# Kernel optimization log

Measured on AMD Instinct MI355X. Metric: run time of the kernel, lower is better.

The kernel has to match this reference:

```python
import jax, jax.numpy as jnp
import numpy as np

NUM_HEADS = 4


def setup_inputs() -> dict:
    key = jax.random.key(0)
    ks = jax.random.split(key, 14)
    B, T, N, Fin, Fout, E = 4, 16, 1000, 64, 128, 12000
    s_in = 1.0 / np.sqrt(Fin)
    s_out = 1.0 / np.sqrt(Fout)
    return {
        "x": jax.random.normal(ks[0], (B, T, N, Fin), jnp.float32),
        "edge_index": jax.random.randint(ks[1], (2, E), 0, N, dtype=jnp.int64),
        # per-gate ChebConv weights (gate order: z, r, h); W0 = self term, W1 = neighbor term
        "wx0": jax.random.normal(ks[2], (3, Fin, Fout), jnp.float32) * s_in,
        "wx1": jax.random.normal(ks[3], (3, Fin, Fout), jnp.float32) * s_in,
        "bx": jax.random.normal(ks[4], (3, Fout), jnp.float32) * 0.01,
        "wh0": jax.random.normal(ks[5], (3, Fout, Fout), jnp.float32) * s_out,
        "wh1": jax.random.normal(ks[6], (3, Fout, Fout), jnp.float32) * s_out,
        "bh": jax.random.normal(ks[7], (3, Fout), jnp.float32) * 0.01,
        # torch nn.MultiheadAttention params
        "w_in": jax.random.normal(ks[8], (3 * Fout, Fout), jnp.float32) * s_out,
        "b_in": jax.random.normal(ks[9], (3 * Fout,), jnp.float32) * 0.01,
        "w_out": jax.random.normal(ks[10], (Fout, Fout), jnp.float32) * s_out,
        "b_out": jax.random.normal(ks[11], (Fout,), jnp.float32) * 0.01,
    }


def reference(x, edge_index, wx0, wx1, bx, wh0, wh1, bh, w_in, b_in, w_out, b_out):
    B, T, N, Fin = x.shape
    Fout = wx0.shape[-1]
    H = NUM_HEADS
    Dh = Fout // H
    L = B * T
    row, col = edge_index[0], edge_index[1]

    # symmetric normalization  D^{-1/2} A D^{-1/2}
    deg = jax.ops.segment_sum(jnp.ones(row.shape, x.dtype), row, num_segments=N)
    dinv = jnp.where(deg > 0, 1.0 / jnp.sqrt(jnp.maximum(deg, 1.0)), 0.0)
    normw = dinv[row] * dinv[col]  # [E]

    # [B,T,N,F] -> [N, T*B, F]  (time-major merge, matching x.view in torch)
    xg = x.transpose(2, 1, 0, 3).reshape(N, T * B, Fin)

    def conv(z, W0, W1, b):
        # ChebConv-style: self transform + sym-normalized 1-hop aggregation
        agg = jax.ops.segment_sum(normw[:, None, None] * z[col], row, num_segments=N)
        return z @ W0 + agg @ W1 + b

    # single GConvGRU step with H0 = 0
    h0 = jnp.zeros((N, T * B, Fout), x.dtype)
    Z = jax.nn.sigmoid(conv(xg, wx0[0], wx1[0], bx[0]) + conv(h0, wh0[0], wh1[0], bh[0]))
    R = jax.nn.sigmoid(conv(xg, wx0[1], wx1[1], bx[1]) + conv(h0, wh0[1], wh1[1], bh[1]))
    Ht = jnp.tanh(conv(xg, wx0[2], wx1[2], bx[2]) + conv(h0 * R, wh0[2], wh1[2], bh[2]))
    Hn = Z * h0 + (1.0 - Z) * Ht  # [N, T*B, Fout]

    # [N,T*B,F] -> [B*T, N, F]  (torch MHA layout: L=B*T, batch=N)
    a = Hn.reshape(N, T, B, Fout).transpose(2, 1, 0, 3).reshape(L, N, Fout)
    qkv = a @ w_in.T + b_in
    q, k, v = jnp.split(qkv, 3, axis=-1)

    def heads(t):
        return t.reshape(L, N, H, Dh).transpose(1, 2, 0, 3)  # [N,H,L,Dh]

    q, k, v = heads(q), heads(k), heads(v)
    att = jax.nn.softmax(jnp.einsum('nhld,nhmd->nhlm', q, k) / np.sqrt(Dh).astype(x.dtype), axis=-1)
    ctx = jnp.einsum('nhlm,nhmd->nhld', att, v).transpose(2, 0, 1, 3).reshape(L, N, Fout)
    out = ctx @ w_out.T + b_out
    return out.reshape(B, T, N, Fout)
```

## Files before the change

### kernel.cpp

```cpp
#include <hip/hip_runtime.h>
#include <math.h>

#define Nn 1000

#define OFF_ROWPTR 0
#define OFF_CSCOL  2048
#define OFF_CSW    18432
#define OFF_WCAT   34816
#define OFF_BC     67584
#define OFF_WTIN   67840
#define OFF_WTOUT  116992
#define OFF_XGAT   133376
#define OFF_Q      8325376
#define OFF_KV     16517376
#define OFF_END    32901376

__global__ __launch_bounds__(1024)
void k_csr(const void* edge, int E, int* rowptr_g, int* cs_col, float* cs_w) {
  __shared__ int deg[1000];
  __shared__ int rp[1001];
  __shared__ int fill[1000];
  __shared__ float dinv[1000];
  __shared__ int sflag;
  __shared__ int sc[1024];
  const int tid = threadIdx.x;
  if (tid == 0) {
    const long long* p = (const long long*)edge;
    int ok = 1;
    for (int i = 0; i < 16; ++i) { long long v = p[i]; if (v < 0 || v >= Nn) ok = 0; }
    sflag = ok;
  }
  for (int i = tid; i < 1000; i += 1024) { deg[i] = 0; fill[i] = 0; }
  __syncthreads();
  const int fl = sflag;
  for (int e = tid; e < E; e += 1024) {
    int r = fl ? (int)((const long long*)edge)[e] : ((const int*)edge)[e];
    atomicAdd(&deg[r], 1);
  }
  __syncthreads();
  sc[tid] = (tid < 1000) ? deg[tid] : 0;
  __syncthreads();
  for (int off = 1; off < 1024; off <<= 1) {
    int t = (tid >= off) ? sc[tid - off] : 0;
    __syncthreads();
    sc[tid] += t;
    __syncthreads();
  }
  if (tid == 0) { rp[0] = 0; rowptr_g[0] = 0; }
  if (tid < 1000) {
    rp[tid + 1] = sc[tid];
    rowptr_g[tid + 1] = sc[tid];
    float d = (float)deg[tid];
    dinv[tid] = (d > 0.f) ? (1.0f / sqrtf(d)) : 0.f;
  }
  __syncthreads();
  for (int e = tid; e < E; e += 1024) {
    int r = fl ? (int)((const long long*)edge)[e] : ((const int*)edge)[e];
    int c = fl ? (int)((const long long*)edge)[E + e] : ((const int*)edge)[E + e];
    int pos = rp[r] + atomicAdd(&fill[r], 1);
    cs_col[pos] = c;
    cs_w[pos] = dinv[r] * dinv[c];
  }
}

__global__ __launch_bounds__(256)
void k_prep(const float* __restrict__ x,
            const float* __restrict__ wx0, const float* __restrict__ wx1,
            const float* __restrict__ bx, const float* __restrict__ bh,
            const float* __restrict__ w_in, const float* __restrict__ w_out,
            float* __restrict__ ws) {
  const int bid = blockIdx.x;
  const int tid = threadIdx.x;
  if (bid < 1000) {
    __shared__ float tile[64][65];
    const int n = bid;
    const int f = tid & 63;
    #pragma unroll
    for (int i = 0; i < 16; ++i) {
      const int bt = (tid >> 6) + i * 4;
      const int l = (bt & 15) * 4 + (bt >> 4);
      tile[f][l] = x[(bt * 1000 + n) * 64 + f];
    }
    __syncthreads();
    const int l = tid & 63;
    #pragma unroll
    for (int i = 0; i < 16; ++i) {
      const int fo = (tid >> 6) + i * 4;
      ws[OFF_XGAT + n * 4096 + fo * 64 + l] = tile[fo][l];
    }
    return;
  }
  int idx = (bid - 1000) * 256 + tid;
  if (idx < 32768) {
    int f = idx >> 8, j = idx & 255;
    int g = (j < 128) ? 0 : 2, jj = j & 127;
    float v = (f < 64) ? wx0[(g * 64 + f) * 128 + jj]
                       : wx1[(g * 64 + (f - 64)) * 128 + jj];
    ws[OFF_WCAT + idx] = v;
    return;
  }
  idx -= 32768;
  if (idx < 256) {
    int g = (idx < 128) ? 0 : 2, jj = idx & 127;
    ws[OFF_BC + idx] = bx[g * 128 + jj] + bh[g * 128 + jj];
    return;
  }
  idx -= 256;
  if (idx < 49152) {
    int f = idx / 384, j = idx % 384;
    ws[OFF_WTIN + idx] = w_in[j * 128 + f];
    return;
  }
  idx -= 49152;
  if (idx < 16384) {
    int f = idx >> 7, j = idx & 127;
    ws[OFF_WTOUT + idx] = w_out[j * 128 + f];
  }
}

__global__ __launch_bounds__(256, 4)
void k_fused2(const float* __restrict__ ws, const int* __restrict__ wsi,
              float* __restrict__ out,
              const float* __restrict__ b_in, const float* __restrict__ b_out,
              float* __restrict__ qs_base, float* __restrict__ kv_base) {
  __shared__ float lds[8192];
  const int n = blockIdx.x;
  const int tid = threadIdx.x;
  float* __restrict__ qs = qs_base + (size_t)n * 8192;
  float* __restrict__ kv = kv_base + (size_t)n * 16384;

  {
    const float4* xsrc = reinterpret_cast<const float4*>(ws + OFF_XGAT + n * 4096);
    #pragma unroll
    for (int i = 0; i < 4; ++i)
      *reinterpret_cast<float4*>(lds + 4096 + i * 1024 + tid * 4) = xsrc[i * 256 + tid];
    float4 acc[4];
    #pragma unroll
    for (int i = 0; i < 4; ++i) { acc[i].x = 0.f; acc[i].y = 0.f; acc[i].z = 0.f; acc[i].w = 0.f; }
    const int kb = wsi[OFF_ROWPTR + n], ke = wsi[OFF_ROWPTR + n + 1];
    for (int k = kb; k < ke; ++k) {
      const int c = wsi[OFF_CSCOL + k];
      const float wgt = ws[OFF_CSW + k];
      const float4* src = reinterpret_cast<const float4*>(ws + OFF_XGAT + c * 4096);
      #pragma unroll
      for (int i = 0; i < 4; ++i) {
        const float4 v = src[i * 256 + tid];
        acc[i].x = fmaf(wgt, v.x, acc[i].x);
        acc[i].y = fmaf(wgt, v.y, acc[i].y);
        acc[i].z = fmaf(wgt, v.z, acc[i].z);
        acc[i].w = fmaf(wgt, v.w, acc[i].w);
      }
    }
    #pragma unroll
    for (int i = 0; i < 4; ++i)
      *reinterpret_cast<float4*>(lds + i * 1024 + tid * 4) = acc[i];
  }
  __syncthreads();

  const int ry = tid >> 5, tx = tid & 31;
  const int r0 = ry * 8, j0 = tx * 4;

  {
    float accz[8][4], acch[8][4];
    #pragma unroll
    for (int c = 0; c < 4; ++c) {
      const float bz = ws[OFF_BC + j0 + c];
      const float bhv = ws[OFF_BC + 128 + j0 + c];
      #pragma unroll
      for (int r = 0; r < 8; ++r) { accz[r][c] = bz; acch[r][c] = bhv; }
    }
    const float* Wc = ws + OFF_WCAT;
    #pragma unroll 2
    for (int f = 0; f < 128; ++f) {
      const int base = (f < 64) ? (4096 + f * 64) : ((f - 64) * 64);
      const float4 a0 = *reinterpret_cast<const float4*>(lds + base + r0);
      const float4 a1 = *reinterpret_cast<const float4*>(lds + base + r0 + 4);
      const float4 wz = *reinterpret_cast<const float4*>(Wc + f * 256 + j0);
      const float4 wh = *reinterpret_cast<const float4*>(Wc + f * 256 + 128 + j0);
      const float av[8] = {a0.x, a0.y, a0.z, a0.w, a1.x, a1.y, a1.z, a1.w};
      const float wzv[4] = {wz.x, wz.y, wz.z, wz.w};
      const float whv[4] = {wh.x, wh.y, wh.z, wh.w};
      #pragma unroll
      for (int r = 0; r < 8; ++r)
        #pragma unroll
        for (int c = 0; c < 4; ++c) {
          accz[r][c] = fmaf(av[r], wzv[c], accz[r][c]);
          acch[r][c] = fmaf(av[r], whv[c], acch[r][c]);
        }
    }
    __syncthreads();
    #pragma unroll
    for (int r = 0; r < 8; ++r) {
      const int l = r0 + r;
      const int lp = (l & 3) * 16 + (l >> 2);
      float4 v;
      const float z0 = 1.0f / (1.0f + __expf(-accz[r][0]));
      const float z1 = 1.0f / (1.0f + __expf(-accz[r][1]));
      const float z2 = 1.0f / (1.0f + __expf(-accz[r][2]));
      const float z3 = 1.0f / (1.0f + __expf(-accz[r][3]));
      v.x = (1.0f - z0) * tanhf(acch[r][0]);
      v.y = (1.0f - z1) * tanhf(acch[r][1]);
      v.z = (1.0f - z2) * tanhf(acch[r][2]);
      v.w = (1.0f - z3) * tanhf(acch[r][3]);
      *reinterpret_cast<float4*>(lds + lp * 128 + j0) = v;
    }
  }
  __syncthreads();

  {
    const float* Wt = ws + OFF_WTIN;
    #pragma unroll
    for (int g = 0; g < 3; ++g) {
      float acc[8][4];
      #pragma unroll
      for (int c = 0; c < 4; ++c) {
        const float b = b_in[g * 128 + j0 + c];
        #pragma unroll
        for (int r = 0; r < 8; ++r) acc[r][c] = b;
      }
      #pragma unroll 1
      for (int fc = 0; fc < 32; ++fc) {
        float av[8][4];
        #pragma unroll
        for (int r = 0; r < 8; ++r)
          *reinterpret_cast<float4*>(av[r]) =
              *reinterpret_cast<const float4*>(lds + (r0 + r) * 128 + fc * 4);
        #pragma unroll
        for (int i = 0; i < 4; ++i) {
          const float4 w4 = *reinterpret_cast<const float4*>(Wt + (fc * 4 + i) * 384 + g * 128 + j0);
          const float wv[4] = {w4.x, w4.y, w4.z, w4.w};
          #pragma unroll
          for (int r = 0; r < 8; ++r)
            #pragma unroll
            for (int c = 0; c < 4; ++c)
              acc[r][c] = fmaf(av[r][i], wv[c], acc[r][c]);
        }
      }
      if (g == 0) {
        #pragma unroll
        for (int r = 0; r < 8; ++r)
          #pragma unroll
          for (int c = 0; c < 4; ++c)
            qs[(j0 + c) * 64 + (r0 + r)] = acc[r][c];
      } else {
        float* dst = kv + (g - 1) * 8192;
        #pragma unroll
        for (int r = 0; r < 8; ++r) {
          float4 v;
          v.x = acc[r][0]; v.y = acc[r][1]; v.z = acc[r][2]; v.w = acc[r][3];
          *reinterpret_cast<float4*>(dst + (r0 + r) * 128 + j0) = v;
        }
      }
    }
  }
  __syncthreads();

  {
    const int h = tid >> 6, l = tid & 63;
    float q[32];
    #pragma unroll
    for (int d = 0; d < 32; ++d)
      q[d] = qs[(h * 32 + d) * 64 + l] * 0.17677669529663687f;
    float den = 0.f;
    float cx[32];
    #pragma unroll
    for (int d = 0; d < 32; ++d) cx[d] = 0.f;
    #pragma unroll 2
    for (int m = 0; m < 64; ++m) {
      const float* kr = kv + m * 128 + h * 32;
      float s0 = 0.f, s1 = 0.f, s2 = 0.f, s3 = 0.f;
      #pragma unroll
      for (int i = 0; i < 8; ++i) {
        const float4 kvv = *reinterpret_cast<const float4*>(kr + i * 4);
        s0 = fmaf(q[i * 4 + 0], kvv.x, s0);
        s1 = fmaf(q[i * 4 + 1], kvv.y, s1);
        s2 = fmaf(q[i * 4 + 2], kvv.z, s2);
        s3 = fmaf(q[i * 4 + 3], kvv.w, s3);
      }
      const float p = __expf((s0 + s1) + (s2 + s3));
      den += p;
      const float* vr = kv + 8192 + m * 128 + h * 32;
      #pragma unroll
      for (int i = 0; i < 8; ++i) {
        const float4 vv = *reinterpret_cast<const float4*>(vr + i * 4);
        cx[i * 4 + 0] = fmaf(p, vv.x, cx[i * 4 + 0]);
        cx[i * 4 + 1] = fmaf(p, vv.y, cx[i * 4 + 1]);
        cx[i * 4 + 2] = fmaf(p, vv.z, cx[i * 4 + 2]);
        cx[i * 4 + 3] = fmaf(p, vv.w, cx[i * 4 + 3]);
      }
    }
    const float inv = 1.0f / den;
    const int ms = (l & 7) << 2;
    #pragma unroll
    for (int i = 0; i < 8; ++i) {
      float4 v;
      v.x = cx[i * 4 + 0] * inv; v.y = cx[i * 4 + 1] * inv;
      v.z = cx[i * 4 + 2] * inv; v.w = cx[i * 4 + 3] * inv;
      *reinterpret_cast<float4*>(lds + l * 128 + ((h * 32 + i * 4) ^ ms)) = v;
    }
  }
  __syncthreads();

  {
    float acc[8][4];
    #pragma unroll
    for (int c = 0; c < 4; ++c) {
      const float b = b_out[j0 + c];
      #pragma unroll
      for (int r = 0; r < 8; ++r) acc[r][c] = b;
    }
    const float* Wt = ws + OFF_WTOUT;
    #pragma unroll 1
    for (int fc = 0; fc < 32; ++fc) {
      float av[8][4];
      #pragma unroll
      for (int r = 0; r < 8; ++r) {
        const int row = r0 + r;
        const int ms = (row & 7) << 2;
        *reinterpret_cast<float4*>(av[r]) =
            *reinterpret_cast<const float4*>(lds + row * 128 + ((fc * 4) ^ ms));
      }
      #pragma unroll
      for (int i = 0; i < 4; ++i) {
        const float4 w4 = *reinterpret_cast<const float4*>(Wt + (fc * 4 + i) * 128 + j0);
        const float wv[4] = {w4.x, w4.y, w4.z, w4.w};
        #pragma unroll
        for (int r = 0; r < 8; ++r)
          #pragma unroll
          for (int c = 0; c < 4; ++c)
            acc[r][c] = fmaf(av[r][i], wv[c], acc[r][c]);
      }
    }
    #pragma unroll
    for (int r = 0; r < 8; ++r) {
      float4 v;
      v.x = acc[r][0]; v.y = acc[r][1]; v.z = acc[r][2]; v.w = acc[r][3];
      *reinterpret_cast<float4*>(out + ((size_t)((r0 + r) * 1000 + n)) * 128 + j0) = v;
    }
  }
}

__global__ __launch_bounds__(1024, 1)
void k_fused(const float* __restrict__ ws, const int* __restrict__ wsi,
             float* __restrict__ out,
             const float* __restrict__ b_in, const float* __restrict__ b_out) {
  extern __shared__ float lds[];
  float* R_X = lds;
  float* R_A = lds + 8192;
  float* R_K = lds + 16384;
  float* R_V = lds + 24576;
  float* WL  = lds + 16384;
  const int n = blockIdx.x;
  const int tid = threadIdx.x;
  const int lane = tid & 63;
  const int w = tid >> 6;

  {
    const int f = tid >> 4, l4 = tid & 15;
    const float4 xv = *reinterpret_cast<const float4*>(ws + OFF_XGAT + n * 4096 + f * 64 + l4 * 4);
    *reinterpret_cast<float4*>(R_X + f * 64 + l4 * 4) = xv;
    const int kb = wsi[OFF_ROWPTR + n], ke = wsi[OFF_ROWPTR + n + 1];
    float4 acc = {0.f, 0.f, 0.f, 0.f};
    for (int k = kb; k < ke; ++k) {
      const int c = wsi[OFF_CSCOL + k];
      const float wgt = ws[OFF_CSW + k];
      const float4 v = *reinterpret_cast<const float4*>(ws + OFF_XGAT + c * 4096 + f * 64 + l4 * 4);
      acc.x = fmaf(wgt, v.x, acc.x);
      acc.y = fmaf(wgt, v.y, acc.y);
      acc.z = fmaf(wgt, v.z, acc.z);
      acc.w = fmaf(wgt, v.w, acc.w);
    }
    *reinterpret_cast<float4*>(R_X + (64 + f) * 64 + l4 * 4) = acc;
  }
  __syncthreads();

  {
    float accz[8], acch[8];
    #pragma unroll
    for (int c = 0; c < 8; ++c) {
      accz[c] = ws[OFF_BC + w * 8 + c];
      acch[c] = ws[OFF_BC + 128 + w * 8 + c];
    }
    for (int ch = 0; ch < 2; ++ch) {
      const float4* src = reinterpret_cast<const float4*>(ws + OFF_WCAT + ch * 16384);
      float4* dst = reinterpret_cast<float4*>(WL);
      #pragma unroll
      for (int i = 0; i < 4; ++i) dst[tid + i * 1024] = src[tid + i * 1024];
      __syncthreads();
      #pragma unroll 4
      for (int f0 = 0; f0 < 64; ++f0) {
        const float av = R_X[(ch * 64 + f0) * 64 + lane];
        const float4 wz0 = *reinterpret_cast<const float4*>(WL + f0 * 256 + w * 8);
        const float4 wz1 = *reinterpret_cast<const float4*>(WL + f0 * 256 + w * 8 + 4);
        const float4 wh0 = *reinterpret_cast<const float4*>(WL + f0 * 256 + 128 + w * 8);
        const float4 wh1 = *reinterpret_cast<const float4*>(WL + f0 * 256 + 128 + w * 8 + 4);
        accz[0] = fmaf(av, wz0.x, accz[0]); accz[1] = fmaf(av, wz0.y, accz[1]);
        accz[2] = fmaf(av, wz0.z, accz[2]); accz[3] = fmaf(av, wz0.w, accz[3]);
        accz[4] = fmaf(av, wz1.x, accz[4]); accz[5] = fmaf(av, wz1.y, accz[5]);
        accz[6] = fmaf(av, wz1.z, accz[6]); accz[7] = fmaf(av, wz1.w, accz[7]);
        acch[0] = fmaf(av, wh0.x, acch[0]); acch[1] = fmaf(av, wh0.y, acch[1]);
        acch[2] = fmaf(av, wh0.z, acch[2]); acch[3] = fmaf(av, wh0.w, acch[3]);
        acch[4] = fmaf(av, wh1.x, acch[4]); acch[5] = fmaf(av, wh1.y, acch[5]);
        acch[6] = fmaf(av, wh1.z, acch[6]); acch[7] = fmaf(av, wh1.w, acch[7]);
      }
      __syncthreads();
    }
    #pragma unroll
    for (int c = 0; c < 8; ++c) {
      const float z = 1.0f / (1.0f + __expf(-accz[c]));
      const float hn = (1.0f - z) * tanhf(acch[c]);
      R_A[(w * 8 + c) * 64 + lane] = hn;
    }
  }
  __syncthreads();

  {
    float acc[24];
    const int j0 = w * 24;
    #pragma unroll
    for (int c = 0; c < 24; ++c) acc[c] = b_in[j0 + c];
    for (int ch = 0; ch < 4; ++ch) {
      const float4* src = reinterpret_cast<const float4*>(ws + OFF_WTIN + ch * 12288);
      float4* dst = reinterpret_cast<float4*>(WL);
      #pragma unroll
      for (int i = 0; i < 3; ++i) dst[tid + i * 1024] = src[tid + i * 1024];
      __syncthreads();
      #pragma unroll 2
      for (int f0 = 0; f0 < 32; ++f0) {
        const float av = R_A[(ch * 32 + f0) * 64 + lane];
        #pragma unroll
        for (int c6 = 0; c6 < 6; ++c6) {
          const float4 wv = *reinterpret_cast<const float4*>(WL + f0 * 384 + j0 + c6 * 4);
          acc[c6 * 4 + 0] = fmaf(av, wv.x, acc[c6 * 4 + 0]);
          acc[c6 * 4 + 1] = fmaf(av, wv.y, acc[c6 * 4 + 1]);
          acc[c6 * 4 + 2] = fmaf(av, wv.z, acc[c6 * 4 + 2]);
          acc[c6 * 4 + 3] = fmaf(av, wv.w, acc[c6 * 4 + 3]);
        }
      }
      __syncthreads();
    }
    const int sw = (lane & 7) << 2;
    #pragma unroll
    for (int c = 0; c < 24; ++c) {
      const int j = j0 + c;
      if (j < 128)      R_X[j * 64 + lane] = acc[c];
      else if (j < 256) R_K[lane * 128 + ((j - 128) ^ sw)] = acc[c];
      else              R_V[lane * 128 + ((j - 256) ^ sw)] = acc[c];
    }
  }
  __syncthreads();

  if (tid < 256) {
    const int h = tid >> 6, l = tid & 63;
    float q[32];
    #pragma unroll
    for (int d = 0; d < 32; ++d)
      q[d] = R_X[(h * 32 + d) * 64 + l] * 0.17677669529663687f;
    float den = 0.f;
    float cx[32];
    #pragma unroll
    for (int d = 0; d < 32; ++d) cx[d] = 0.f;
    for (int m = 0; m < 64; ++m) {
      const int sw = (m & 7) << 2;
      const float* kr = R_K + m * 128;
      float s0 = 0.f, s1 = 0.f, s2 = 0.f, s3 = 0.f;
      #pragma unroll
      for (int i = 0; i < 8; ++i) {
        const float4 kvv = *reinterpret_cast<const float4*>(kr + ((h * 32 + i * 4) ^ sw));
        s0 = fmaf(q[i * 4 + 0], kvv.x, s0);
        s1 = fmaf(q[i * 4 + 1], kvv.y, s1);
        s2 = fmaf(q[i * 4 + 2], kvv.z, s2);
        s3 = fmaf(q[i * 4 + 3], kvv.w, s3);
      }
      const float p = __expf((s0 + s1) + (s2 + s3));
      den += p;
      const float* vr = R_V + m * 128;
      #pragma unroll
      for (int i = 0; i < 8; ++i) {
        const float4 vv = *reinterpret_cast<const float4*>(vr + ((h * 32 + i * 4) ^ sw));
        cx[i * 4 + 0] = fmaf(p, vv.x, cx[i * 4 + 0]);
        cx[i * 4 + 1] = fmaf(p, vv.y, cx[i * 4 + 1]);
        cx[i * 4 + 2] = fmaf(p, vv.z, cx[i * 4 + 2]);
        cx[i * 4 + 3] = fmaf(p, vv.w, cx[i * 4 + 3]);
      }
    }
    const float inv = 1.0f / den;
    #pragma unroll
    for (int d = 0; d < 32; ++d)
      R_A[(h * 32 + d) * 64 + l] = cx[d] * inv;
  }
  __syncthreads();

  {
    float acc[8];
    #pragma unroll
    for (int c = 0; c < 8; ++c) acc[c] = b_out[w * 8 + c];
    {
      const float4* src = reinterpret_cast<const float4*>(ws + OFF_WTOUT);
      float4* dst = reinterpret_cast<float4*>(WL);
      #pragma unroll
      for (int i = 0; i < 4; ++i) dst[tid + i * 1024] = src[tid + i * 1024];
    }
    __syncthreads();
    #pragma unroll 4
    for (int f = 0; f < 128; ++f) {
      const float av = R_A[f * 64 + lane];
      const float4 w0 = *reinterpret_cast<const float4*>(WL + f * 128 + w * 8);
      const float4 w1 = *reinterpret_cast<const float4*>(WL + f * 128 + w * 8 + 4);
      acc[0] = fmaf(av, w0.x, acc[0]); acc[1] = fmaf(av, w0.y, acc[1]);
      acc[2] = fmaf(av, w0.z, acc[2]); acc[3] = fmaf(av, w0.w, acc[3]);
      acc[4] = fmaf(av, w1.x, acc[4]); acc[5] = fmaf(av, w1.y, acc[5]);
      acc[6] = fmaf(av, w1.z, acc[6]); acc[7] = fmaf(av, w1.w, acc[7]);
    }
    __syncthreads();
    float4 o0 = {acc[0], acc[1], acc[2], acc[3]};
    float4 o1 = {acc[4], acc[5], acc[6], acc[7]};
    *reinterpret_cast<float4*>(WL + lane * 132 + w * 8) = o0;
    *reinterpret_cast<float4*>(WL + lane * 132 + w * 8 + 4) = o1;
  }
  __syncthreads();

  {
    const int l = tid >> 4, j8 = tid & 15;
    const int lpp = (l & 3) * 16 + (l >> 2);
    const float4 a = *reinterpret_cast<const float4*>(WL + l * 132 + j8 * 8);
    const float4 b = *reinterpret_cast<const float4*>(WL + l * 132 + j8 * 8 + 4);
    float* dst = out + ((size_t)(lpp * 1000 + n)) * 128 + j8 * 8;
    *reinterpret_cast<float4*>(dst) = a;
    *reinterpret_cast<float4*>(dst + 4) = b;
  }
}

extern "C" void kernel_launch(void* const* d_in, const int* in_sizes, int n_in,
                              void* d_out, int out_size, void* d_ws, size_t ws_size,
                              hipStream_t stream) {
  const float* x     = (const float*)d_in[0];
  const void*  edge  = d_in[1];
  const float* wx0   = (const float*)d_in[2];
  const float* wx1   = (const float*)d_in[3];
  const float* bx    = (const float*)d_in[4];
  const float* bh    = (const float*)d_in[7];
  const float* w_in  = (const float*)d_in[8];
  const float* b_in  = (const float*)d_in[9];
  const float* w_out = (const float*)d_in[10];
  const float* b_out = (const float*)d_in[11];
  float* out = (float*)d_out;
  float* ws  = (float*)d_ws;
  int*   wsi = (int*)d_ws;
  const int E = in_sizes[1] / 2;

  k_csr<<<1, 1024, 0, stream>>>(edge, E, wsi + OFF_ROWPTR,
                                wsi + OFF_CSCOL, ws + OFF_CSW);
  k_prep<<<1385, 256, 0, stream>>>(x, wx0, wx1, bx, bh, w_in, w_out, ws);

  if (ws_size >= (size_t)OFF_END * 4) {
    k_fused2<<<1000, 256, 0, stream>>>(ws, wsi, out, b_in, b_out,
                                       ws + OFF_Q, ws + OFF_KV);
  } else {
    (void)hipFuncSetAttribute((const void*)k_fused,
                              hipFuncAttributeMaxDynamicSharedMemorySize, 131072);
    k_fused<<<1000, 1024, 131072, stream>>>(ws, wsi, out, b_in, b_out);
  }
}
```

Measured before the change: 402.9 us.

## Compute K/V projections tile-by-tile into LDS instead of global scratch

The K and V projections are no longer written to a global scratch buffer and read back during attention. They are now produced eight rows at a time into a small LDS tile and consumed right away, interleaved with the attention loop, which removes the global KV round trip and its workspace. The Hn tile in LDS also gets an XOR swizzle to reduce bank conflicts on the row reads. In exchange, LDS per block grows by 8 KB and each block runs extra barriers across eight tile iterations, and the K/V projection uses a thinner per-thread tile with less register reuse.

```diff
diff --git a/kernel.cpp b/kernel.cpp
--- a/kernel.cpp
+++ b/kernel.cpp
@@ -12,8 +12,7 @@
 #define OFF_WTOUT  116992
 #define OFF_XGAT   133376
 #define OFF_Q      8325376
-#define OFF_KV     16517376
-#define OFF_END    32901376
+#define OFF_QEND   16517376
 
 __global__ __launch_bounds__(1024)
 void k_csr(const void* edge, int E, int* rowptr_g, int* cs_col, float* cs_w) {
@@ -119,15 +118,14 @@
 }
 
 __global__ __launch_bounds__(256, 4)
-void k_fused2(const float* __restrict__ ws, const int* __restrict__ wsi,
+void k_fused3(const float* __restrict__ ws, const int* __restrict__ wsi,
               float* __restrict__ out,
               const float* __restrict__ b_in, const float* __restrict__ b_out,
-              float* __restrict__ qs_base, float* __restrict__ kv_base) {
-  __shared__ float lds[8192];
+              float* __restrict__ qs_base) {
+  __shared__ float lds[10240];
   const int n = blockIdx.x;
   const int tid = threadIdx.x;
   float* __restrict__ qs = qs_base + (size_t)n * 8192;
-  float* __restrict__ kv = kv_base + (size_t)n * 16384;
 
   {
     const float4* xsrc = reinterpret_cast<const float4*>(ws + OFF_XGAT + n * 4096);
@@ -202,101 +200,136 @@
       v.y = (1.0f - z1) * tanhf(acch[r][1]);
       v.z = (1.0f - z2) * tanhf(acch[r][2]);
       v.w = (1.0f - z3) * tanhf(acch[r][3]);
-      *reinterpret_cast<float4*>(lds + lp * 128 + j0) = v;
+      *reinterpret_cast<float4*>(lds + lp * 128 + (j0 ^ ((lp & 7) << 2))) = v;
     }
   }
   __syncthreads();
 
   {
     const float* Wt = ws + OFF_WTIN;
-    #pragma unroll
-    for (int g = 0; g < 3; ++g) {
-      float acc[8][4];
-      #pragma unroll
-      for (int c = 0; c < 4; ++c) {
-        const float b = b_in[g * 128 + j0 + c];
-        #pragma unroll
-        for (int r = 0; r < 8; ++r) acc[r][c] = b;
-      }
-      #pragma unroll 1
-      for (int fc = 0; fc < 32; ++fc) {
-        float av[8][4];
-        #pragma unroll
-        for (int r = 0; r < 8; ++r)
-          *reinterpret_cast<float4*>(av[r]) =
-              *reinterpret_cast<const float4*>(lds + (r0 + r) * 128 + fc * 4);
-        #pragma unroll
-        for (int i = 0; i < 4; ++i) {
-          const float4 w4 = *reinterpret_cast<const float4*>(Wt + (fc * 4 + i) * 384 + g * 128 + j0);
-          const float wv[4] = {w4.x, w4.y, w4.z, w4.w};
-          #pragma unroll
-          for (int r = 0; r < 8; ++r)
-            #pragma unroll
-            for (int c = 0; c < 4; ++c)
-              acc[r][c] = fmaf(av[r][i], wv[c], acc[r][c]);
-        }
-      }
-      if (g == 0) {
+    float acc[8][4];
+    #pragma unroll
+    for (int c = 0; c < 4; ++c) {
+      const float b = b_in[j0 + c];
+      #pragma unroll
+      for (int r = 0; r < 8; ++r) acc[r][c] = b;
+    }
+    #pragma unroll 1
+    for (int fc = 0; fc < 32; ++fc) {
+      float av[8][4];
+      #pragma unroll
+      for (int r = 0; r < 8; ++r)
+        *reinterpret_cast<float4*>(av[r]) =
+            *reinterpret_cast<const float4*>(lds + (r0 + r) * 128 + ((fc * 4) ^ (r << 2)));
+      #pragma unroll
+      for (int i = 0; i < 4; ++i) {
+        const float4 w4 = *reinterpret_cast<const float4*>(Wt + (fc * 4 + i) * 384 + j0);
+        const float wv[4] = {w4.x, w4.y, w4.z, w4.w};
         #pragma unroll
         for (int r = 0; r < 8; ++r)
           #pragma unroll
           for (int c = 0; c < 4; ++c)
-            qs[(j0 + c) * 64 + (r0 + r)] = acc[r][c];
-      } else {
-        float* dst = kv + (g - 1) * 8192;
-        #pragma unroll
-        for (int r = 0; r < 8; ++r) {
-          float4 v;
-          v.x = acc[r][0]; v.y = acc[r][1]; v.z = acc[r][2]; v.w = acc[r][3];
-          *reinterpret_cast<float4*>(dst + (r0 + r) * 128 + j0) = v;
+            acc[r][c] = fmaf(av[r][i], wv[c], acc[r][c]);
+      }
+    }
+    #pragma unroll
+    for (int r = 0; r < 8; ++r)
+      #pragma unroll
+      for (int c = 0; c < 4; ++c)
+        qs[(j0 + c) * 64 + (r0 + r)] = acc[r][c];
+  }
+  __syncthreads();
+
+  const int h = tid >> 6, lq = tid & 63;
+  float q[32];
+  #pragma unroll
+  for (int d = 0; d < 32; ++d)
+    q[d] = qs[(h * 32 + d) * 64 + lq] * 0.17677669529663687f;
+
+  float den = 0.f;
+  float cx[32];
+  #pragma unroll
+  for (int d = 0; d < 32; ++d) cx[d] = 0.f;
+
+  const int mat = tid >> 7;
+  const int rq = (tid >> 5) & 3;
+  const int j4 = (tid & 31) * 4;
+  float* kvls = lds + 8192;
+
+  for (int kt = 0; kt < 8; ++kt) {
+    if (kt) __syncthreads();
+    {
+      const int m0 = kt * 8;
+      const int mmA = rq * 2, mmB = mmA + 1;
+      float accA[4], accB[4];
+      #pragma unroll
+      for (int c = 0; c < 4; ++c) {
+        const float b = b_in[128 + mat * 128 + j4 + c];
+        accA[c] = b; accB[c] = b;
+      }
+      const float* Wt = ws + OFF_WTIN;
+      #pragma unroll 1
+      for (int fc = 0; fc < 32; ++fc) {
+        float avA[4], avB[4];
+        *reinterpret_cast<float4*>(avA) =
+            *reinterpret_cast<const float4*>(lds + (m0 + mmA) * 128 + ((fc * 4) ^ ((mmA & 7) << 2)));
+        *reinterpret_cast<float4*>(avB) =
+            *reinterpret_cast<const float4*>(lds + (m0 + mmB) * 128 + ((fc * 4) ^ ((mmB & 7) << 2)));
+        #pragma unroll
+        for (int i = 0; i < 4; ++i) {
+          const float4 w4 = *reinterpret_cast<const float4*>(Wt + (fc * 4 + i) * 384 + 128 + mat * 128 + j4);
+          const float wv[4] = {w4.x, w4.y, w4.z, w4.w};
+          #pragma unroll
+          for (int c = 0; c < 4; ++c) {
+            accA[c] = fmaf(avA[i], wv[c], accA[c]);
+            accB[c] = fmaf(avB[i], wv[c], accB[c]);
+          }
         }
       }
-    }
-  }
-  __syncthreads();
-
-  {
-    const int h = tid >> 6, l = tid & 63;
-    float q[32];
-    #pragma unroll
-    for (int d = 0; d < 32; ++d)
-      q[d] = qs[(h * 32 + d) * 64 + l] * 0.17677669529663687f;
-    float den = 0.f;
-    float cx[32];
-    #pragma unroll
-    for (int d = 0; d < 32; ++d) cx[d] = 0.f;
-    #pragma unroll 2
-    for (int m = 0; m < 64; ++m) {
-      const float* kr = kv + m * 128 + h * 32;
-      float s0 = 0.f, s1 = 0.f, s2 = 0.f, s3 = 0.f;
-      #pragma unroll
-      for (int i = 0; i < 8; ++i) {
-        const float4 kvv = *reinterpret_cast<const float4*>(kr + i * 4);
-        s0 = fmaf(q[i * 4 + 0], kvv.x, s0);
-        s1 = fmaf(q[i * 4 + 1], kvv.y, s1);
-        s2 = fmaf(q[i * 4 + 2], kvv.z, s2);
-        s3 = fmaf(q[i * 4 + 3], kvv.w, s3);
-      }
-      const float p = __expf((s0 + s1) + (s2 + s3));
-      den += p;
-      const float* vr = kv + 8192 + m * 128 + h * 32;
-      #pragma unroll
-      for (int i = 0; i < 8; ++i) {
-        const float4 vv = *reinterpret_cast<const float4*>(vr + i * 4);
-        cx[i * 4 + 0] = fmaf(p, vv.x, cx[i * 4 + 0]);
-        cx[i * 4 + 1] = fmaf(p, vv.y, cx[i * 4 + 1]);
-        cx[i * 4 + 2] = fmaf(p, vv.z, cx[i * 4 + 2]);
-        cx[i * 4 + 3] = fmaf(p, vv.w, cx[i * 4 + 3]);
-      }
-    }
+      float* dst = kvls + mat * 1024;
+      float4 vA = {accA[0], accA[1], accA[2], accA[3]};
+      float4 vB = {accB[0], accB[1], accB[2], accB[3]};
+      *reinterpret_cast<float4*>(dst + mmA * 128 + (j4 ^ ((mmA & 3) << 2))) = vA;
+      *reinterpret_cast<float4*>(dst + mmB * 128 + (j4 ^ ((mmB & 3) << 2))) = vB;
+    }
+    __syncthreads();
+    {
+      #pragma unroll
+      for (int mm = 0; mm < 8; ++mm) {
+        const int swk = (mm & 3) << 2;
+        const float* kr = kvls + mm * 128;
+        float s0 = 0.f, s1 = 0.f, s2 = 0.f, s3 = 0.f;
+        #pragma unroll
+        for (int i = 0; i < 8; ++i) {
+          const float4 kv = *reinterpret_cast<const float4*>(kr + ((h * 32 + i * 4) ^ swk));
+          s0 = fmaf(q[i * 4 + 0], kv.x, s0);
+          s1 = fmaf(q[i * 4 + 1], kv.y, s1);
+          s2 = fmaf(q[i * 4 + 2], kv.z, s2);
+          s3 = fmaf(q[i * 4 + 3], kv.w, s3);
+        }
+        const float p = __expf((s0 + s1) + (s2 + s3));
+        den += p;
+        const float* vr = kvls + 1024 + mm * 128;
+        #pragma unroll
+        for (int i = 0; i < 8; ++i) {
+          const float4 vv = *reinterpret_cast<const float4*>(vr + ((h * 32 + i * 4) ^ swk));
+          cx[i * 4 + 0] = fmaf(p, vv.x, cx[i * 4 + 0]);
+          cx[i * 4 + 1] = fmaf(p, vv.y, cx[i * 4 + 1]);
+          cx[i * 4 + 2] = fmaf(p, vv.z, cx[i * 4 + 2]);
+          cx[i * 4 + 3] = fmaf(p, vv.w, cx[i * 4 + 3]);
+        }
+      }
+    }
+  }
+  {
     const float inv = 1.0f / den;
-    const int ms = (l & 7) << 2;
+    const int ms = (lq & 7) << 2;
     #pragma unroll
     for (int i = 0; i < 8; ++i) {
       float4 v;
       v.x = cx[i * 4 + 0] * inv; v.y = cx[i * 4 + 1] * inv;
       v.z = cx[i * 4 + 2] * inv; v.w = cx[i * 4 + 3] * inv;
-      *reinterpret_cast<float4*>(lds + l * 128 + ((h * 32 + i * 4) ^ ms)) = v;
+      *reinterpret_cast<float4*>(lds + lq * 128 + ((h * 32 + i * 4) ^ ms)) = v;
     }
   }
   __syncthreads();
@@ -314,12 +347,9 @@
     for (int fc = 0; fc < 32; ++fc) {
       float av[8][4];
       #pragma unroll
-      for (int r = 0; r < 8; ++r) {
-        const int row = r0 + r;
-        const int ms = (row & 7) << 2;
+      for (int r = 0; r < 8; ++r)
         *reinterpret_cast<float4*>(av[r]) =
-            *reinterpret_cast<const float4*>(lds + row * 128 + ((fc * 4) ^ ms));
-      }
+            *reinterpret_cast<const float4*>(lds + (r0 + r) * 128 + ((fc * 4) ^ (r << 2)));
       #pragma unroll
       for (int i = 0; i < 4; ++i) {
         const float4 w4 = *reinterpret_cast<const float4*>(Wt + (fc * 4 + i) * 128 + j0);
@@ -553,9 +583,8 @@
                                 wsi + OFF_CSCOL, ws + OFF_CSW);
   k_prep<<<1385, 256, 0, stream>>>(x, wx0, wx1, bx, bh, w_in, w_out, ws);
 
-  if (ws_size >= (size_t)OFF_END * 4) {
-    k_fused2<<<1000, 256, 0, stream>>>(ws, wsi, out, b_in, b_out,
-                                       ws + OFF_Q, ws + OFF_KV);
+  if (ws_size >= (size_t)OFF_QEND * 4) {
+    k_fused3<<<1000, 256, 0, stream>>>(ws, wsi, out, b_in, b_out, ws + OFF_Q);
   } else {
     (void)hipFuncSetAttribute((const void*)k_fused,
                               hipFuncAttributeMaxDynamicSharedMemorySize, 131072);
```

Result: no change. 401.5 us (-0.3%).
